# Performance work log

Measured on AMD Instinct MI355X. Metric: run time of the kernel, lower is better.

Reference implementation:

```python
import jax, jax.numpy as jnp
import numpy as np

N = 50000
DIM = 768   # input_dim == feature dim (self.L)
D_ATT = 128 # self.D


def setup_inputs() -> dict:
    key = jax.random.key(0)
    ks = jax.random.split(key, 6)
    s = lambda fan_in: 1.0 / np.sqrt(fan_in)
    return {
        "x": jax.random.normal(ks[0], (1, N, DIM), dtype=jnp.float32),
        "W_feat": jax.random.normal(ks[1], (DIM, DIM), dtype=jnp.float32) * s(DIM),
        "b_feat": jax.random.normal(ks[2], (DIM,), dtype=jnp.float32) * s(DIM),
        "W_a": jax.random.normal(ks[3], (D_ATT, DIM), dtype=jnp.float32) * s(DIM),
        "W_b": jax.random.normal(ks[4], (D_ATT, DIM), dtype=jnp.float32) * s(DIM),
        "W_c": jax.random.normal(ks[5], (1, D_ATT), dtype=jnp.float32) * s(D_ATT),
    }


def reference(x, W_feat, b_feat, W_a, W_b, W_c):
    # x: [1, N, DIM] -> squeeze bag dim -> [N, DIM]
    h = jax.nn.relu(jnp.einsum('nd,ed->ne', x[0], W_feat) + b_feat)  # [N, 768]
    a = jax.nn.relu(jnp.einsum('nd,kd->nk', h, W_a))      # [N, 128]
    b = jax.nn.sigmoid(jnp.einsum('nd,kd->nk', h, W_b))   # [N, 128]
    logits = jnp.einsum('nk,ok->on', a * b, W_c)           # [1, N] (transpose fused)
    A = jax.nn.softmax(logits, axis=-1)                    # [1, N]
    return jnp.einsum('on,nd->od', A, h)                   # [1, 768]
```

## Files before the change

kernel.cpp:

```cpp
#include <hip/hip_runtime.h>
#include <hip/hip_bf16.h>
#include <stdint.h>

#define DEVINL __device__ __forceinline__

using bf16x8 = __attribute__((ext_vector_type(8))) short;
using f32x4  = __attribute__((ext_vector_type(4))) float;

static constexpr int NPTS = 50000;
static constexpr int NPAD = 50048;
static constexpr int DIM  = 768;
static constexpr int DATT = 128;
static constexpr int NRB  = NPAD / 128;

DEVINL ushort f2b(float f) {
  uint32_t u = __float_as_uint(f);
  u += 0x7fffu + ((u >> 16) & 1u);
  return (ushort)(u >> 16);
}
DEVINL float b2f(ushort u) { return __uint_as_float(((uint32_t)u) << 16); }

DEVINL void gload_lds16(const void* g, void* l) {
  __builtin_amdgcn_global_load_lds((const __attribute__((address_space(1))) void*)g,
                                   (__attribute__((address_space(3))) void*)l,
                                   16, 0, 0);
}

__global__ void cvt8_kernel(const float* __restrict__ src, ushort* __restrict__ dst,
                            int n8_src, int n8_dst) {
  const int stride = gridDim.x * blockDim.x;
  for (int i = blockIdx.x * blockDim.x + threadIdx.x; i < n8_dst; i += stride) {
    float4 v0 = {0.f, 0.f, 0.f, 0.f}, v1 = {0.f, 0.f, 0.f, 0.f};
    if (i < n8_src) {
      const float4* s4 = (const float4*)src;
      v0 = s4[(long)i * 2];
      v1 = s4[(long)i * 2 + 1];
    }
    ushort4 o0 = { f2b(v0.x), f2b(v0.y), f2b(v0.z), f2b(v0.w) };
    ushort4 o1 = { f2b(v1.x), f2b(v1.y), f2b(v1.z), f2b(v1.w) };
    ((ushort4*)dst)[(long)i * 2]     = o0;
    ((ushort4*)dst)[(long)i * 2 + 1] = o1;
  }
}

__global__ void cvt_weights_kernel(const float* __restrict__ Wf, const float* __restrict__ Wa,
                                   const float* __restrict__ Wb,
                                   ushort* __restrict__ wfb, ushort* __restrict__ wab,
                                   ushort* __restrict__ wbb) {
  const int NF = DIM * DIM / 8, NA = DATT * DIM / 8;
  int i = blockIdx.x * blockDim.x + threadIdx.x;
  const float* src; ushort* dst; int j;
  if (i < NF)               { src = Wf; dst = wfb; j = i; }
  else if (i < NF + NA)     { src = Wa; dst = wab; j = i - NF; }
  else if (i < NF + 2 * NA) { src = Wb; dst = wbb; j = i - NF - NA; }
  else return;
  const float4* s4 = (const float4*)src;
  float4 v0 = s4[(long)j * 2];
  float4 v1 = s4[(long)j * 2 + 1];
  ushort4 o0 = { f2b(v0.x), f2b(v0.y), f2b(v0.z), f2b(v0.w) };
  ushort4 o1 = { f2b(v1.x), f2b(v1.y), f2b(v1.z), f2b(v1.w) };
  ((ushort4*)dst)[(long)j * 2]     = o0;
  ((ushort4*)dst)[(long)j * 2 + 1] = o1;
}

__global__ __launch_bounds__(512)
void gemm_h_kernel(const ushort* __restrict__ A, const ushort* __restrict__ B,
                   const float* __restrict__ bias, ushort* __restrict__ H) {
  __shared__ ushort As[128 * 64];
  __shared__ ushort Bs[256 * 64];
  const int tid  = threadIdx.x;
  const int wid  = tid >> 6;
  const int lane = tid & 63;

  const int nwg = NRB * 3;
  const int q = nwg >> 3, r = nwg & 7;
  const int xcd = blockIdx.x & 7, idx = blockIdx.x >> 3;
  const int wgid = (xcd < r ? xcd * (q + 1) : r * (q + 1) + (xcd - r) * q) + idx;
  const int row0 = (wgid / 3) * 128;
  const int col0 = (wgid % 3) * 256;

  const int wrow = (wid >> 2) * 64;
  const int wcol = (wid & 3) * 64;

  f32x4 acc[4][4] = {};

  const int ld_r = lane >> 3;
  const int ld_c = (lane & 7) * 8;

  for (int k0 = 0; k0 < DIM; k0 += 64) {
    __syncthreads();
#pragma unroll
    for (int i = 0; i < 2; ++i) {
      const int ch = i * 8 + wid;
      gload_lds16(A + (long)(row0 + ch * 8 + ld_r) * DIM + k0 + ld_c, As + ch * 512);
    }
#pragma unroll
    for (int i = 0; i < 4; ++i) {
      const int ch = i * 8 + wid;
      gload_lds16(B + (long)(col0 + ch * 8 + ld_r) * DIM + k0 + ld_c, Bs + ch * 512);
    }
    __syncthreads();
#pragma unroll
    for (int kk = 0; kk < 2; ++kk) {
      const int kc = kk * 32 + (lane >> 4) * 8;
      bf16x8 a[4];
#pragma unroll
      for (int m = 0; m < 4; ++m)
        a[m] = *(const bf16x8*)(As + (wrow + m * 16 + (lane & 15)) * 64 + kc);
#pragma unroll
      for (int n = 0; n < 4; ++n) {
        bf16x8 b = *(const bf16x8*)(Bs + (wcol + n * 16 + (lane & 15)) * 64 + kc);
#pragma unroll
        for (int m = 0; m < 4; ++m)
          acc[m][n] = __builtin_amdgcn_mfma_f32_16x16x32_bf16(a[m], b, acc[m][n], 0, 0, 0);
      }
    }
  }

  const int lq = lane >> 4;
  const int lc = lane & 15;
#pragma unroll
  for (int n = 0; n < 4; ++n) {
    const int cg = col0 + wcol + n * 16 + lc;
    const float bv = bias[cg];
#pragma unroll
    for (int m = 0; m < 4; ++m) {
      const int rg = row0 + wrow + m * 16 + lq * 4;
#pragma unroll
      for (int r2 = 0; r2 < 4; ++r2) {
        float v = acc[m][n][r2] + bv;
        v = fmaxf(v, 0.0f);
        H[(long)(rg + r2) * DIM + cg] = f2b(v);
      }
    }
  }
}

__global__ __launch_bounds__(512)
void gate_kernel(const ushort* __restrict__ Hm, const ushort* __restrict__ Wa,
                 const ushort* __restrict__ Wb, const float* __restrict__ Wc,
                 float* __restrict__ logits) {
  __shared__ ushort Hs [128 * 64];
  __shared__ ushort Was[128 * 64];
  __shared__ ushort Wbs[128 * 64];
  const int tid  = threadIdx.x;
  const int wid  = tid >> 6;
  const int lane = tid & 63;
  const int row0 = blockIdx.x * 128;

  f32x4 fa[8] = {};
  f32x4 fb[8] = {};

  const int ld_r = lane >> 3;
  const int ld_c = (lane & 7) * 8;

  for (int k0 = 0; k0 < DIM; k0 += 64) {
    __syncthreads();
#pragma unroll
    for (int i = 0; i < 2; ++i) {
      const int ch = i * 8 + wid;
      const int r  = ch * 8 + ld_r;
      gload_lds16(Hm + (long)(row0 + r) * DIM + k0 + ld_c, Hs  + ch * 512);
      gload_lds16(Wa + (long)r * DIM        + k0 + ld_c, Was + ch * 512);
      gload_lds16(Wb + (long)r * DIM        + k0 + ld_c, Wbs + ch * 512);
    }
    __syncthreads();
#pragma unroll
    for (int kk = 0; kk < 2; ++kk) {
      const int kc = kk * 32 + (lane >> 4) * 8;
      bf16x8 h = *(const bf16x8*)(Hs + (wid * 16 + (lane & 15)) * 64 + kc);
#pragma unroll
      for (int n = 0; n < 8; ++n) {
        bf16x8 wa = *(const bf16x8*)(Was + (n * 16 + (lane & 15)) * 64 + kc);
        bf16x8 wb = *(const bf16x8*)(Wbs + (n * 16 + (lane & 15)) * 64 + kc);
        fa[n] = __builtin_amdgcn_mfma_f32_16x16x32_bf16(h, wa, fa[n], 0, 0, 0);
        fb[n] = __builtin_amdgcn_mfma_f32_16x16x32_bf16(h, wb, fb[n], 0, 0, 0);
      }
    }
  }

  const int lc = lane & 15;
  const int lq = lane >> 4;
  float g[4];
#pragma unroll
  for (int r = 0; r < 4; ++r) {
    float s = 0.f;
#pragma unroll
    for (int n = 0; n < 8; ++n) {
      float av = fmaxf(fa[n][r], 0.f);
      float sg = 1.f / (1.f + expf(-fb[n][r]));
      s += av * sg * Wc[n * 16 + lc];
    }
    s += __shfl_xor(s, 1);
    s += __shfl_xor(s, 2);
    s += __shfl_xor(s, 4);
    s += __shfl_xor(s, 8);
    g[r] = s;
  }
  if (lc == 0) {
    const int rbase = row0 + wid * 16 + lq * 4;
#pragma unroll
    for (int r = 0; r < 4; ++r) {
      const int nidx = rbase + r;
      if (nidx < NPTS) logits[nidx] = g[r];
    }
  }
}

__global__ __launch_bounds__(1024)
void softmax_stats_kernel(const float* __restrict__ logits, float* __restrict__ stats) {
  __shared__ float red[1024];
  const int tid = threadIdx.x;
  float m = -1e30f;
  for (int i = tid; i < NPTS; i += 1024) m = fmaxf(m, logits[i]);
  red[tid] = m; __syncthreads();
  for (int s = 512; s > 0; s >>= 1) {
    if (tid < s) red[tid] = fmaxf(red[tid], red[tid + s]);
    __syncthreads();
  }
  m = red[0];
  __syncthreads();
  float sum = 0.f;
  for (int i = tid; i < NPTS; i += 1024) sum += expf(logits[i] - m);
  red[tid] = sum; __syncthreads();
  for (int s = 512; s > 0; s >>= 1) {
    if (tid < s) red[tid] += red[tid + s];
    __syncthreads();
  }
  if (tid == 0) { stats[0] = m; stats[1] = red[0]; }
}

__global__ __launch_bounds__(192)
void weighted_partial_kernel(const ushort* __restrict__ Hm, const float* __restrict__ logits,
                             const float* __restrict__ stats, float* __restrict__ part) {
  __shared__ float w[128];
  const int b = blockIdx.x, tid = threadIdx.x;
  const int n0 = b * 128;
  if (tid < 128) {
    const int n = n0 + tid;
    w[tid] = (n < NPTS) ? expf(logits[n] - stats[0]) : 0.f;
  }
  __syncthreads();
  float4 acc = {0.f, 0.f, 0.f, 0.f};
  const ushort* hp = Hm + (long)n0 * DIM + tid * 4;
#pragma unroll 4
  for (int r = 0; r < 128; ++r) {
    const float wr = w[r];
    ushort4 v = *(const ushort4*)(hp + (long)r * DIM);
    acc.x += wr * b2f(v.x);
    acc.y += wr * b2f(v.y);
    acc.z += wr * b2f(v.z);
    acc.w += wr * b2f(v.w);
  }
  ((float4*)(part + (long)b * DIM))[tid] = acc;
}

__global__ void final_reduce_kernel(const float* __restrict__ part,
                                    const float* __restrict__ stats,
                                    float* __restrict__ out) {
  const int c = blockIdx.x * blockDim.x + threadIdx.x;
  if (c >= DIM) return;
  float s = 0.f;
  for (int b = 0; b < NRB; ++b) s += part[(long)b * DIM + c];
  out[c] = s / stats[1];
}

extern "C" void kernel_launch(void* const* d_in, const int* in_sizes, int n_in,
                              void* d_out, int out_size, void* d_ws, size_t ws_size,
                              hipStream_t stream) {
  const float* x  = (const float*)d_in[0];
  const float* Wf = (const float*)d_in[1];
  const float* bf = (const float*)d_in[2];
  const float* Wa = (const float*)d_in[3];
  const float* Wb = (const float*)d_in[4];
  const float* Wc = (const float*)d_in[5];
  float* out = (float*)d_out;

  char* p = (char*)d_ws;
  ushort* xb  = (ushort*)p; p += (size_t)NPAD * DIM * 2;
  ushort* hb  = (ushort*)p; p += (size_t)NPAD * DIM * 2;
  ushort* wfb = (ushort*)p; p += (size_t)DIM * DIM * 2;
  ushort* wab = (ushort*)p; p += (size_t)DATT * DIM * 2;
  ushort* wbb = (ushort*)p; p += (size_t)DATT * DIM * 2;
  float* logits = (float*)p; p += (size_t)NPAD * 4;
  float* stats  = (float*)p; p += 256;
  float* part   = (float*)p; p += (size_t)NRB * DIM * 4;

  cvt8_kernel<<<2048, 256, 0, stream>>>(x, xb, NPTS * DIM / 8, NPAD * DIM / 8);
  cvt_weights_kernel<<<384, 256, 0, stream>>>(Wf, Wa, Wb, wfb, wab, wbb);

  gemm_h_kernel<<<NRB * 3, 512, 0, stream>>>(xb, wfb, bf, hb);
  gate_kernel<<<NRB, 512, 0, stream>>>(hb, wab, wbb, Wc, logits);
  softmax_stats_kernel<<<1, 1024, 0, stream>>>(logits, stats);
  weighted_partial_kernel<<<NRB, 192, 0, stream>>>(hb, logits, stats, part);
  final_reduce_kernel<<<3, 256, 0, stream>>>(part, stats, out);
}
```

Measured before the change: 234.3 us.

## Pipeline H GEMM with 256x256 tiles, swizzled LDS, split softmax stats

The feature GEMM moves to 256x256 tiles with a four-buffer LDS ring fed two k-steps ahead by async global-to-LDS loads. It also uses an XOR-swizzled LDS layout, explicit vmcnt waits, and raised wave priority around the MFMA bursts, so loads overlap compute and LDS bank conflicts drop. NPAD is raised to 50176 so rows are a multiple of 256, which makes the grid 588 blocks. The single-block softmax statistics kernel is split into a 49-block partial reduction plus a one-wave combine to spread the max/sum work across the GPU. The price is more padded rows and a fragile hand-written wait count and pipeline schedule.

```diff
diff --git a/kernel.cpp b/kernel.cpp
--- a/kernel.cpp
+++ b/kernel.cpp
@@ -8,10 +8,11 @@
 using f32x4  = __attribute__((ext_vector_type(4))) float;
 
 static constexpr int NPTS = 50000;
-static constexpr int NPAD = 50048;
+static constexpr int NPAD = 50176;
 static constexpr int DIM  = 768;
 static constexpr int DATT = 128;
 static constexpr int NRB  = NPAD / 128;
+static constexpr int NSMB = 49;
 
 DEVINL ushort f2b(float f) {
   uint32_t u = __float_as_uint(f);
@@ -66,71 +67,109 @@
 __global__ __launch_bounds__(512)
 void gemm_h_kernel(const ushort* __restrict__ A, const ushort* __restrict__ B,
                    const float* __restrict__ bias, ushort* __restrict__ H) {
-  __shared__ ushort As[128 * 64];
-  __shared__ ushort Bs[256 * 64];
+  __shared__ __align__(16) char lds[4][32768];
+
   const int tid  = threadIdx.x;
   const int wid  = tid >> 6;
   const int lane = tid & 63;
 
-  const int nwg = NRB * 3;
-  const int q = nwg >> 3, r = nwg & 7;
-  const int xcd = blockIdx.x & 7, idx = blockIdx.x >> 3;
-  const int wgid = (xcd < r ? xcd * (q + 1) : r * (q + 1) + (xcd - r) * q) + idx;
-  const int row0 = (wgid / 3) * 128;
+  const int bid = blockIdx.x;
+  const int xcd = bid & 7, idx = bid >> 3;
+  const int wgid = (xcd < 4 ? xcd * 74 : 4 * 74 + (xcd - 4) * 73) + idx;
+  const int row0 = (wgid / 3) * 256;
   const int col0 = (wgid % 3) * 256;
 
-  const int wrow = (wid >> 2) * 64;
-  const int wcol = (wid & 3) * 64;
-
-  f32x4 acc[4][4] = {};
-
-  const int ld_r = lane >> 3;
-  const int ld_c = (lane & 7) * 8;
-
-  for (int k0 = 0; k0 < DIM; k0 += 64) {
-    __syncthreads();
-#pragma unroll
-    for (int i = 0; i < 2; ++i) {
-      const int ch = i * 8 + wid;
-      gload_lds16(A + (long)(row0 + ch * 8 + ld_r) * DIM + k0 + ld_c, As + ch * 512);
-    }
-#pragma unroll
-    for (int i = 0; i < 4; ++i) {
-      const int ch = i * 8 + wid;
-      gload_lds16(B + (long)(col0 + ch * 8 + ld_r) * DIM + k0 + ld_c, Bs + ch * 512);
-    }
-    __syncthreads();
-#pragma unroll
-    for (int kk = 0; kk < 2; ++kk) {
-      const int kc = kk * 32 + (lane >> 4) * 8;
-      bf16x8 a[4];
-#pragma unroll
-      for (int m = 0; m < 4; ++m)
-        a[m] = *(const bf16x8*)(As + (wrow + m * 16 + (lane & 15)) * 64 + kc);
-#pragma unroll
-      for (int n = 0; n < 4; ++n) {
-        bf16x8 b = *(const bf16x8*)(Bs + (wcol + n * 16 + (lane & 15)) * 64 + kc);
-#pragma unroll
-        for (int m = 0; m < 4; ++m)
-          acc[m][n] = __builtin_amdgcn_mfma_f32_16x16x32_bf16(a[m], b, acc[m][n], 0, 0, 0);
-      }
-    }
+  const ushort* Abase = A + (long)row0 * DIM;
+  const ushort* Bbase = B + (long)col0 * DIM;
+
+  const int pre = (lane & 7) ^ (lane >> 3);
+  const int sr0 = wid * 16 + ((lane >> 3) << 1) + (pre >> 2);
+  const int sc0 = (pre & 3) * 8;
+
+  auto STAGE_A = [&](int tt) {
+    const int buf = tt & 3;
+    const long k0 = (long)tt * 32;
+#pragma unroll
+    for (int i = 0; i < 2; ++i)
+      gload_lds16(Abase + (long)(i * 128 + sr0) * DIM + k0 + sc0,
+                  &lds[buf][(i * 64 + wid * 8) * 128]);
+  };
+  auto STAGE_B = [&](int tt) {
+    const int buf = tt & 3;
+    const long k0 = (long)tt * 32;
+#pragma unroll
+    for (int i = 0; i < 2; ++i)
+      gload_lds16(Bbase + (long)(i * 128 + sr0) * DIM + k0 + sc0,
+                  &lds[buf][16384 + (i * 64 + wid * 8) * 128]);
+  };
+
+  f32x4 acc0[4][4] = {};
+  f32x4 acc1[4][4] = {};
+
+  const int wrbase = (wid >> 2) * 128;
+  const int wcbase = (wid & 3) * 64;
+
+  auto PHASE = [&](int t, int ch, f32x4 (&ac)[4][4]) {
+    const int buf = t & 3;
+    const ushort* Ab = (const ushort*)&lds[buf][0];
+    const ushort* Bb = (const ushort*)&lds[buf][16384];
+    const int j = lane >> 4;
+    bf16x8 a[4], b[4];
+#pragma unroll
+    for (int fm = 0; fm < 4; ++fm) {
+      const int ra = wrbase + ch * 64 + fm * 16 + (lane & 15);
+      const int pr = ra >> 1;
+      const int sl = (j + 4 * (ra & 1)) ^ (pr & 7);
+      a[fm] = *(const bf16x8*)(Ab + pr * 64 + sl * 8);
+    }
+#pragma unroll
+    for (int fn = 0; fn < 4; ++fn) {
+      const int rb = wcbase + fn * 16 + (lane & 15);
+      const int pr = rb >> 1;
+      const int sl = (j + 4 * (rb & 1)) ^ (pr & 7);
+      b[fn] = *(const bf16x8*)(Bb + pr * 64 + sl * 8);
+    }
+    if (t < 22) { if (ch == 0) STAGE_A(t + 2); else STAGE_B(t + 2); }
+    __builtin_amdgcn_sched_barrier(0);
+    __builtin_amdgcn_s_setprio(1);
+#pragma unroll
+    for (int fn = 0; fn < 4; ++fn)
+#pragma unroll
+      for (int fm = 0; fm < 4; ++fm)
+        ac[fm][fn] = __builtin_amdgcn_mfma_f32_16x16x32_bf16(a[fm], b[fn], ac[fm][fn], 0, 0, 0);
+    __builtin_amdgcn_s_setprio(0);
+    __builtin_amdgcn_sched_barrier(0);
+  };
+
+  STAGE_A(0); STAGE_B(0); STAGE_A(1); STAGE_B(1);
+
+#pragma unroll 1
+  for (int t = 0; t < 24; ++t) {
+    if (t < 23) asm volatile("s_waitcnt vmcnt(4)" ::: "memory");
+    else        asm volatile("s_waitcnt vmcnt(0)" ::: "memory");
+    __builtin_amdgcn_s_barrier();
+    PHASE(t, 0, acc0);
+    if (t < 23) asm volatile("s_waitcnt vmcnt(4)" ::: "memory");
+    else        asm volatile("s_waitcnt vmcnt(0)" ::: "memory");
+    __builtin_amdgcn_s_barrier();
+    PHASE(t, 1, acc1);
   }
 
   const int lq = lane >> 4;
   const int lc = lane & 15;
 #pragma unroll
-  for (int n = 0; n < 4; ++n) {
-    const int cg = col0 + wcol + n * 16 + lc;
+  for (int fn = 0; fn < 4; ++fn) {
+    const int cg = col0 + wcbase + fn * 16 + lc;
     const float bv = bias[cg];
 #pragma unroll
-    for (int m = 0; m < 4; ++m) {
-      const int rg = row0 + wrow + m * 16 + lq * 4;
+    for (int fm = 0; fm < 4; ++fm) {
+      const int rg0 = row0 + wrbase + fm * 16 + lq * 4;
 #pragma unroll
       for (int r2 = 0; r2 < 4; ++r2) {
-        float v = acc[m][n][r2] + bv;
-        v = fmaxf(v, 0.0f);
-        H[(long)(rg + r2) * DIM + cg] = f2b(v);
+        float v0 = acc0[fm][fn][r2] + bv;
+        H[(long)(rg0 + r2) * DIM + cg] = f2b(fmaxf(v0, 0.0f));
+        float v1 = acc1[fm][fn][r2] + bv;
+        H[(long)(rg0 + 64 + r2) * DIM + cg] = f2b(fmaxf(v1, 0.0f));
       }
     }
   }
@@ -208,26 +247,37 @@
 }
 
 __global__ __launch_bounds__(1024)
-void softmax_stats_kernel(const float* __restrict__ logits, float* __restrict__ stats) {
+void softmax_part_kernel(const float* __restrict__ logits, float* __restrict__ part2) {
   __shared__ float red[1024];
   const int tid = threadIdx.x;
-  float m = -1e30f;
-  for (int i = tid; i < NPTS; i += 1024) m = fmaxf(m, logits[i]);
-  red[tid] = m; __syncthreads();
+  const int n = blockIdx.x * 1024 + tid;
+  const float v = (n < NPTS) ? logits[n] : -1e30f;
+  red[tid] = v; __syncthreads();
   for (int s = 512; s > 0; s >>= 1) {
     if (tid < s) red[tid] = fmaxf(red[tid], red[tid + s]);
     __syncthreads();
   }
-  m = red[0];
+  const float m = red[0];
   __syncthreads();
-  float sum = 0.f;
-  for (int i = tid; i < NPTS; i += 1024) sum += expf(logits[i] - m);
-  red[tid] = sum; __syncthreads();
+  red[tid] = (n < NPTS) ? expf(v - m) : 0.f;
+  __syncthreads();
   for (int s = 512; s > 0; s >>= 1) {
     if (tid < s) red[tid] += red[tid + s];
     __syncthreads();
   }
-  if (tid == 0) { stats[0] = m; stats[1] = red[0]; }
+  if (tid == 0) { part2[blockIdx.x * 2] = m; part2[blockIdx.x * 2 + 1] = red[0]; }
+}
+
+__global__ void softmax_comb_kernel(const float* __restrict__ part2,
+                                    float* __restrict__ stats) {
+  const int l = threadIdx.x;
+  float m = (l < NSMB) ? part2[l * 2]     : -1e30f;
+  float s = (l < NSMB) ? part2[l * 2 + 1] : 0.f;
+  float M = m;
+  for (int o = 32; o > 0; o >>= 1) M = fmaxf(M, __shfl_xor(M, o));
+  float sc = s * expf(m - M);
+  for (int o = 32; o > 0; o >>= 1) sc += __shfl_xor(sc, o);
+  if (l == 0) { stats[0] = M; stats[1] = sc; }
 }
 
 __global__ __launch_bounds__(192)
@@ -284,14 +334,16 @@
   ushort* wbb = (ushort*)p; p += (size_t)DATT * DIM * 2;
   float* logits = (float*)p; p += (size_t)NPAD * 4;
   float* stats  = (float*)p; p += 256;
+  float* part2  = (float*)p; p += 1024;
   float* part   = (float*)p; p += (size_t)NRB * DIM * 4;
 
   cvt8_kernel<<<2048, 256, 0, stream>>>(x, xb, NPTS * DIM / 8, NPAD * DIM / 8);
   cvt_weights_kernel<<<384, 256, 0, stream>>>(Wf, Wa, Wb, wfb, wab, wbb);
 
-  gemm_h_kernel<<<NRB * 3, 512, 0, stream>>>(xb, wfb, bf, hb);
+  gemm_h_kernel<<<196 * 3, 512, 0, stream>>>(xb, wfb, bf, hb);
   gate_kernel<<<NRB, 512, 0, stream>>>(hb, wab, wbb, Wc, logits);
-  softmax_stats_kernel<<<1, 1024, 0, stream>>>(logits, stats);
+  softmax_part_kernel<<<NSMB, 1024, 0, stream>>>(logits, part2);
+  softmax_comb_kernel<<<1, 64, 0, stream>>>(part2, stats);
   weighted_partial_kernel<<<NRB, 192, 0, stream>>>(hb, logits, stats, part);
   final_reduce_kernel<<<3, 256, 0, stream>>>(part, stats, out);
 }
```

Result: faster. 227.0 us (-3.1%).
